# Kernel tuning notes

Hardware: AMD Instinct MI355X
Metric: run time of the kernel (lower is better)

Reference implementation:

```python
import jax, jax.numpy as jnp
import numpy as np

N_HEAD = 16
HEAD_DIM = 64
NEG_INF = -1e10


def setup_inputs() -> dict:
    key = jax.random.key(0)
    k1, k2, k3 = jax.random.split(key, 3)
    B, S, D = 1, 4096, 1024
    x = jax.random.normal(k1, (B, S, D), dtype=jnp.float32)
    Wqkv = jax.random.normal(k2, (D, 3 * D), dtype=jnp.float32) * 0.02
    bqkv = jnp.zeros((3 * D,), dtype=jnp.float32)
    Wproj = jax.random.normal(k3, (D, D), dtype=jnp.float32) * 0.02
    bproj = jnp.zeros((D,), dtype=jnp.float32)
    return {"x": x, "Wqkv": Wqkv, "bqkv": bqkv, "Wproj": Wproj, "bproj": bproj}


def reference(x, Wqkv, bqkv, Wproj, bproj):
    B, S, D = x.shape
    qkv = x @ Wqkv + bqkv                      # [B, S, 3D]
    q, k, v = jnp.split(qkv, 3, axis=2)
    # split heads -> [B, H, S, Dh]
    def split_heads(t):
        return t.reshape(B, S, N_HEAD, HEAD_DIM).transpose(0, 2, 1, 3)
    q, k, v = split_heads(q), split_heads(k), split_heads(v)
    scale = 1.0 / jnp.sqrt(jnp.float32(HEAD_DIM))
    scores = jnp.einsum('bhqd,bhkd->bhqk', q, k) * scale  # [B, H, S, S]
    causal = jnp.tril(jnp.ones((S, S), dtype=bool))[None, None]
    scores = jnp.where(causal, scores, NEG_INF)
    attn = jax.nn.softmax(scores, axis=-1)
    out = jnp.einsum('bhqk,bhkd->bhqd', attn, v)          # [B, H, S, Dh]
    out = out.transpose(0, 2, 1, 3).reshape(B, S, D)       # merge heads
    return out @ Wproj + bproj
```

## Files before the change

### kernel.cpp

```cpp
#include <hip/hip_runtime.h>
#include <stdint.h>

typedef unsigned short u16;
typedef unsigned u32;
typedef __bf16 bf16x8 __attribute__((ext_vector_type(8)));
typedef float f32x4 __attribute__((ext_vector_type(4)));
typedef u32 u32x4 __attribute__((ext_vector_type(4)));

#define S_LEN 4096
#define D_MODEL 1024
#define NHEAD 16
#define HDIM 64

__device__ __forceinline__ u16 f2bf(float f) {
  unsigned u = __builtin_bit_cast(unsigned, f);
  u += 0x7fffu + ((u >> 16) & 1u);
  return (u16)(u >> 16);
}

__device__ __forceinline__ u32 cvt_pk_bf16(float lo, float hi) {
  u32 r;
  asm("v_cvt_pk_bf16_f32 %0, %1, %2" : "=v"(r) : "v"(lo), "v"(hi));
  return r;
}

__device__ __forceinline__ int swz(int row, int col) {
  return (((col >> 3) ^ (row & 7)) << 3) | (col & 7);
}

__device__ __forceinline__ int sigma64(int s) {
  int a = s >> 4;
  return ((a >> 1) << 5) | (((s >> 2) & 3) << 3) | ((a & 1) << 2) | (s & 3);
}

__device__ __forceinline__ void gload16(const void* g, void* l) {
  auto gp = reinterpret_cast<__attribute__((address_space(1))) void*>(
      reinterpret_cast<uintptr_t>(g));
  auto lp = reinterpret_cast<__attribute__((address_space(3))) void*>(
      static_cast<unsigned>(reinterpret_cast<uintptr_t>(l)));
  __builtin_amdgcn_global_load_lds(gp, lp, 16, 0, 0);
}

__global__ __launch_bounds__(256) void k_conv(const float* __restrict__ in,
                                              u16* __restrict__ out, int n) {
  int i = (blockIdx.x * 256 + threadIdx.x) * 4;
  if (i >= n) return;
  float4 v = *reinterpret_cast<const float4*>(in + i);
  ushort4 o = make_ushort4(f2bf(v.x), f2bf(v.y), f2bf(v.z), f2bf(v.w));
  *reinterpret_cast<ushort4*>(out + i) = o;
}

__global__ __launch_bounds__(256) void k_transpose_conv(const float* __restrict__ in,
                                                        u16* __restrict__ out,
                                                        int R, int C) {
  __shared__ float tile[32][33];
  int c0 = blockIdx.x * 32, r0 = blockIdx.y * 32;
  int tx = threadIdx.x, ty = threadIdx.y;
#pragma unroll
  for (int j = 0; j < 4; ++j)
    tile[ty + j * 8][tx] = in[(size_t)(r0 + ty + j * 8) * C + c0 + tx];
  __syncthreads();
#pragma unroll
  for (int j = 0; j < 4; ++j)
    out[(size_t)(c0 + ty + j * 8) * R + r0 + tx] = f2bf(tile[tx][ty + j * 8]);
}

template <int MODE>
__global__ __launch_bounds__(256) void k_gemm(
    const u16* __restrict__ A, const u16* __restrict__ Bt,
    const float* __restrict__ bias, float* __restrict__ Cf,
    u16* __restrict__ Qd, u16* __restrict__ Kd, u16* __restrict__ Vtd,
    int M, int N, int K) {
  __shared__ __align__(16) u16 lds[2][2 * 128 * 32];
  const int tid = threadIdx.x;
  const int w = tid >> 6, lane = tid & 63;
  const int m0 = blockIdx.y * 128, n0 = blockIdx.x * 128;
  const u16* Atile = A + (size_t)m0 * K;
  const u16* Btile = Bt + (size_t)n0 * K;
  const int r = tid >> 2, c = (tid & 3) * 8;
  const int wm = (w >> 1) * 64, wn = (w & 1) * 64;

  f32x4 acc[4][4] = {};
  const int NT = K / 32;

  {
    const u16* ga = Atile + (size_t)r * K + c;
    const u16* gb = Btile + (size_t)r * K + c;
    u16* lb = lds[0];
    gload16(ga, lb + w * 512);
    gload16(ga + (size_t)64 * K, lb + 2048 + w * 512);
    gload16(gb, lb + 4096 + w * 512);
    gload16(gb + (size_t)64 * K, lb + 4096 + 2048 + w * 512);
  }
  int cur = 0;
  for (int t = 0; t < NT; ++t) {
    __syncthreads();
    if (t + 1 < NT) {
      const u16* ga = Atile + (size_t)r * K + (t + 1) * 32 + c;
      const u16* gb = Btile + (size_t)r * K + (t + 1) * 32 + c;
      u16* lb = lds[cur ^ 1];
      gload16(ga, lb + w * 512);
      gload16(ga + (size_t)64 * K, lb + 2048 + w * 512);
      gload16(gb, lb + 4096 + w * 512);
      gload16(gb + (size_t)64 * K, lb + 4096 + 2048 + w * 512);
    }
    const u16* lA = lds[cur];
    const u16* lB = lds[cur] + 4096;
    bf16x8 af[4], bfv[4];
#pragma unroll
    for (int mi = 0; mi < 4; ++mi)
      af[mi] = *reinterpret_cast<const bf16x8*>(
          lA + (wm + mi * 16 + (lane & 15)) * 32 + (lane >> 4) * 8);
#pragma unroll
    for (int ni = 0; ni < 4; ++ni)
      bfv[ni] = *reinterpret_cast<const bf16x8*>(
          lB + (wn + ni * 16 + (lane & 15)) * 32 + (lane >> 4) * 8);
#pragma unroll
    for (int mi = 0; mi < 4; ++mi)
#pragma unroll
      for (int ni = 0; ni < 4; ++ni)
        acc[mi][ni] = __builtin_amdgcn_mfma_f32_16x16x32_bf16(af[mi], bfv[ni],
                                                              acc[mi][ni], 0, 0, 0);
    cur ^= 1;
  }
#pragma unroll
  for (int mi = 0; mi < 4; ++mi) {
#pragma unroll
    for (int ni = 0; ni < 4; ++ni) {
      int colg = n0 + wn + ni * 16 + (lane & 15);
      float bv = bias[colg];
#pragma unroll
      for (int rr = 0; rr < 4; ++rr) {
        int rowg = m0 + wm + mi * 16 + ((lane >> 4) << 2) + rr;
        float v = acc[mi][ni][rr] + bv;
        if (MODE == 1) {
          Cf[(size_t)rowg * N + colg] = v;
        } else {
          if (colg < D_MODEL) {
            u16 b = f2bf(v * 0.1803368801111f);
            int hh = colg >> 6, dd = colg & 63;
            Qd[((size_t)hh * S_LEN + rowg) * 64 + swz(rowg, dd)] = b;
          } else if (colg < 2 * D_MODEL) {
            u16 b = f2bf(v);
            int cc = colg - D_MODEL;
            int hh = cc >> 6, dd = cc & 63;
            Kd[((size_t)hh * S_LEN + rowg) * 64 + swz(rowg, dd)] = b;
          } else {
            u16 b = f2bf(v);
            int cc = colg - 2 * D_MODEL;
            int hh = cc >> 6, dd = cc & 63;
            int csl = sigma64(rowg & 63);
            Vtd[((size_t)hh * 64 + dd) * S_LEN + (rowg & ~63) + swz(dd, csl)] = b;
          }
        }
      }
    }
  }
}

__global__ __launch_bounds__(256) void k_flash(const u16* __restrict__ Qd,
                                               const u16* __restrict__ Kd,
                                               const u16* __restrict__ Vtd,
                                               u16* __restrict__ Ao) {
  __shared__ __align__(16) u16 Ks[2][64 * 64];
  __shared__ __align__(16) u16 Vs[2][64 * 64];
  const int tid = threadIdx.x, w = tid >> 6, lane = tid & 63;
  const int bid = blockIdx.x;
  const int qt = 63 - (bid >> 4), h = bid & 15;
  const u16* Qh = Qd + (size_t)h * S_LEN * 64;
  const u16* Kh = Kd + (size_t)h * S_LEN * 64;
  const u16* Vh = Vtd + (size_t)h * 64 * S_LEN;
  const int r8 = tid >> 3, c8 = (tid & 7) * 8;
  const int g = lane >> 4, ql = lane & 15;

  {
    const u16* gk = Kh + (size_t)r8 * 64 + c8;
    gload16(gk, Ks[0] + w * 512);
    gload16(gk + 32 * 64, Ks[0] + 2048 + w * 512);
    const u16* gv = Vh + (size_t)r8 * S_LEN + c8;
    gload16(gv, Vs[0] + w * 512);
    gload16(gv + (size_t)32 * S_LEN, Vs[0] + 2048 + w * 512);
  }

  bf16x8 qa[2];
  {
    const int rq = qt * 64 + w * 16 + ql;
#pragma unroll
    for (int kk = 0; kk < 2; ++kk)
      qa[kk] = *reinterpret_cast<const bf16x8*>(
          Qh + (size_t)rq * 64 + swz(rq, kk * 32 + g * 8));
  }

  float m_run = -1e30f, l_part = 0.f;
  f32x4 oacc[4] = {};

  __syncthreads();

  int cur = 0;
  for (int j = 0; j <= qt; ++j) {
    if (j < qt) {
      const u16* gk = Kh + ((size_t)((j + 1) * 64 + r8)) * 64 + c8;
      gload16(gk, Ks[cur ^ 1] + w * 512);
      gload16(gk + 32 * 64, Ks[cur ^ 1] + 2048 + w * 512);
      const u16* gv = Vh + (size_t)r8 * S_LEN + (j + 1) * 64 + c8;
      gload16(gv, Vs[cur ^ 1] + w * 512);
      gload16(gv + (size_t)32 * S_LEN, Vs[cur ^ 1] + 2048 + w * 512);
    }

    f32x4 sacc[4] = {};
#pragma unroll
    for (int kk = 0; kk < 2; ++kk) {
#pragma unroll
      for (int ni = 0; ni < 4; ++ni) {
        const int kvl = ni * 16 + ql;
        bf16x8 kb = *reinterpret_cast<const bf16x8*>(
            Ks[cur] + kvl * 64 + swz(kvl, kk * 32 + g * 8));
        sacc[ni] = __builtin_amdgcn_mfma_f32_16x16x32_bf16(kb, qa[kk], sacc[ni], 0, 0, 0);
      }
    }

    float pvv[4][4];
#pragma unroll
    for (int ni = 0; ni < 4; ++ni)
#pragma unroll
      for (int rr = 0; rr < 4; ++rr) pvv[ni][rr] = sacc[ni][rr];

    if (j == qt) {
      const int qoff = w * 16 + ql;
#pragma unroll
      for (int ni = 0; ni < 4; ++ni)
#pragma unroll
        for (int rr = 0; rr < 4; ++rr)
          if (ni * 16 + g * 4 + rr > qoff) pvv[ni][rr] = -1e30f;
    }

    float mx;
    {
      float a0 = fmaxf(fmaxf(pvv[0][0], pvv[0][1]), fmaxf(pvv[0][2], pvv[0][3]));
      float a1 = fmaxf(fmaxf(pvv[1][0], pvv[1][1]), fmaxf(pvv[1][2], pvv[1][3]));
      float a2 = fmaxf(fmaxf(pvv[2][0], pvv[2][1]), fmaxf(pvv[2][2], pvv[2][3]));
      float a3 = fmaxf(fmaxf(pvv[3][0], pvv[3][1]), fmaxf(pvv[3][2], pvv[3][3]));
      mx = fmaxf(fmaxf(a0, a1), fmaxf(a2, a3));
      mx = fmaxf(mx, __shfl_xor(mx, 16));
      mx = fmaxf(mx, __shfl_xor(mx, 32));
    }

    if (__any(mx > m_run + 8.f)) {
      float mn = fmaxf(m_run, mx);
      float alpha = exp2f(m_run - mn);
      m_run = mn;
      l_part *= alpha;
      float ao[4];
#pragma unroll
      for (int rr = 0; rr < 4; ++rr) ao[rr] = __shfl(alpha, g * 4 + rr);
#pragma unroll
      for (int ni = 0; ni < 4; ++ni)
#pragma unroll
        for (int rr = 0; rr < 4; ++rr) oacc[ni][rr] *= ao[rr];
    }

    u32 pk[4][2];
    {
      float rs = 0.f;
#pragma unroll
      for (int ni = 0; ni < 4; ++ni) {
        float p0 = exp2f(pvv[ni][0] - m_run);
        float p1 = exp2f(pvv[ni][1] - m_run);
        float p2 = exp2f(pvv[ni][2] - m_run);
        float p3 = exp2f(pvv[ni][3] - m_run);
        rs += (p0 + p1) + (p2 + p3);
        pk[ni][0] = cvt_pk_bf16(p0, p1);
        pk[ni][1] = cvt_pk_bf16(p2, p3);
      }
      l_part += rs;
    }

#pragma unroll
    for (int kk2 = 0; kk2 < 2; ++kk2) {
      u32x4 pw = {pk[2 * kk2][0], pk[2 * kk2][1], pk[2 * kk2 + 1][0], pk[2 * kk2 + 1][1]};
      bf16x8 pa = __builtin_bit_cast(bf16x8, pw);
#pragma unroll
      for (int ni = 0; ni < 4; ++ni) {
        const int dd = ni * 16 + ql;
        bf16x8 vb = *reinterpret_cast<const bf16x8*>(
            Vs[cur] + dd * 64 + swz(dd, kk2 * 32 + g * 8));
        oacc[ni] = __builtin_amdgcn_mfma_f32_16x16x32_bf16(pa, vb, oacc[ni], 0, 0, 0);
      }
    }

    __syncthreads();
    cur ^= 1;
  }

  {
    float l = l_part;
    l += __shfl_xor(l, 16);
    l += __shfl_xor(l, 32);
    float inv = 1.f / l;
    float io[4];
#pragma unroll
    for (int rr = 0; rr < 4; ++rr) io[rr] = __shfl(inv, g * 4 + rr);
#pragma unroll
    for (int rr = 0; rr < 4; ++rr) {
      int rowg = qt * 64 + w * 16 + g * 4 + rr;
#pragma unroll
      for (int ni = 0; ni < 4; ++ni) {
        int colg = h * 64 + ni * 16 + ql;
        Ao[(size_t)rowg * D_MODEL + colg] = f2bf(oacc[ni][rr] * io[rr]);
      }
    }
  }
}

extern "C" void kernel_launch(void* const* d_in, const int* in_sizes, int n_in,
                              void* d_out, int out_size, void* d_ws, size_t ws_size,
                              hipStream_t stream) {
  const float* x = (const float*)d_in[0];
  const float* Wqkv = (const float*)d_in[1];
  const float* bqkv = (const float*)d_in[2];
  const float* Wproj = (const float*)d_in[3];
  const float* bproj = (const float*)d_in[4];
  float* out = (float*)d_out;
  char* ws = (char*)d_ws;

  u16* xb = (u16*)(ws);
  u16* aout = (u16*)(ws);
  u16* wqkvt = (u16*)(ws + (size_t)(8 << 20));
  u16* wprojt = (u16*)(ws + (size_t)(14 << 20));
  u16* Qd = (u16*)(ws + (size_t)(16 << 20));
  u16* Kd = (u16*)(ws + (size_t)(24 << 20));
  u16* Vtd = (u16*)(ws + (size_t)(32 << 20));

  if (ws_size < (size_t)(40 << 20)) return;

  k_conv<<<dim3(4096), dim3(256), 0, stream>>>(x, xb, S_LEN * D_MODEL);
  k_transpose_conv<<<dim3(96, 32), dim3(32, 8), 0, stream>>>(Wqkv, wqkvt, D_MODEL,
                                                             3 * D_MODEL);
  k_transpose_conv<<<dim3(32, 32), dim3(32, 8), 0, stream>>>(Wproj, wprojt, D_MODEL,
                                                             D_MODEL);
  k_gemm<0><<<dim3(24, 32), dim3(256), 0, stream>>>(xb, wqkvt, bqkv, nullptr, Qd, Kd,
                                                    Vtd, S_LEN, 3 * D_MODEL, D_MODEL);
  k_flash<<<dim3(1024), dim3(256), 0, stream>>>(Qd, Kd, Vtd, aout);
  k_gemm<1><<<dim3(8, 32), dim3(256), 0, stream>>>(aout, wprojt, bproj, out, nullptr,
                                                   nullptr, nullptr, S_LEN, D_MODEL,
                                                   D_MODEL);
}
```

Baseline: 226.9 us.

## Pair causal query tiles per block and use narrower-N GEMM for projection

The flash kernel now has each block process two query tiles, i and 63-i, sharing the K/V loads for the first i+1 tiles. This balances causal work across 512 uniform blocks instead of 1024 uneven ones. The output projection switches to a new 128x64-tile GEMM that launches 512 blocks instead of 256, for better CU coverage. The trade-off is more registers per thread for the second accumulator set, and only 512 flash blocks, which may cost occupancy.

```diff
diff --git a/kernel.cpp b/kernel.cpp
--- a/kernel.cpp
+++ b/kernel.cpp
@@ -158,6 +158,162 @@
   }
 }
 
+__global__ __launch_bounds__(256) void k_gemm_n64(
+    const u16* __restrict__ A, const u16* __restrict__ Bt,
+    const float* __restrict__ bias, float* __restrict__ Cf,
+    int M, int N, int K) {
+  __shared__ __align__(16) u16 lds[2][(128 + 64) * 32];
+  const int tid = threadIdx.x;
+  const int w = tid >> 6, lane = tid & 63;
+  const int g = lane >> 4, ql = lane & 15;
+  const int m0 = blockIdx.y * 128, n0 = blockIdx.x * 64;
+  const u16* Atile = A + (size_t)m0 * K;
+  const u16* Btile = Bt + (size_t)n0 * K;
+  const int r = tid >> 2, c = (tid & 3) * 8;
+  const int wm = (w >> 1) * 64, wn = (w & 1) * 32;
+
+  f32x4 acc[4][2] = {};
+  const int NT = K / 32;
+
+  {
+    const u16* ga = Atile + (size_t)r * K + c;
+    const u16* gb = Btile + (size_t)r * K + c;
+    u16* lb = lds[0];
+    gload16(ga, lb + w * 512);
+    gload16(ga + (size_t)64 * K, lb + 2048 + w * 512);
+    gload16(gb, lb + 4096 + w * 512);
+  }
+  int cur = 0;
+  for (int t = 0; t < NT; ++t) {
+    __syncthreads();
+    if (t + 1 < NT) {
+      const u16* ga = Atile + (size_t)r * K + (t + 1) * 32 + c;
+      const u16* gb = Btile + (size_t)r * K + (t + 1) * 32 + c;
+      u16* lb = lds[cur ^ 1];
+      gload16(ga, lb + w * 512);
+      gload16(ga + (size_t)64 * K, lb + 2048 + w * 512);
+      gload16(gb, lb + 4096 + w * 512);
+    }
+    const u16* lA = lds[cur];
+    const u16* lB = lds[cur] + 4096;
+    bf16x8 af[4], bfv[2];
+#pragma unroll
+    for (int mi = 0; mi < 4; ++mi)
+      af[mi] = *reinterpret_cast<const bf16x8*>(
+          lA + (wm + mi * 16 + ql) * 32 + g * 8);
+#pragma unroll
+    for (int ni = 0; ni < 2; ++ni)
+      bfv[ni] = *reinterpret_cast<const bf16x8*>(
+          lB + (wn + ni * 16 + ql) * 32 + g * 8);
+#pragma unroll
+    for (int mi = 0; mi < 4; ++mi)
+#pragma unroll
+      for (int ni = 0; ni < 2; ++ni)
+        acc[mi][ni] = __builtin_amdgcn_mfma_f32_16x16x32_bf16(af[mi], bfv[ni],
+                                                              acc[mi][ni], 0, 0, 0);
+    cur ^= 1;
+  }
+#pragma unroll
+  for (int mi = 0; mi < 4; ++mi)
+#pragma unroll
+    for (int ni = 0; ni < 2; ++ni) {
+      int colg = n0 + wn + ni * 16 + ql;
+      float bv = bias[colg];
+#pragma unroll
+      for (int rr = 0; rr < 4; ++rr) {
+        int rowg = m0 + wm + mi * 16 + g * 4 + rr;
+        Cf[(size_t)rowg * N + colg] = acc[mi][ni][rr] + bv;
+      }
+    }
+}
+
+__device__ __forceinline__ void flash_tile(const u16* __restrict__ Ksb,
+                                           const u16* __restrict__ Vsb,
+                                           bf16x8 qa0, bf16x8 qa1,
+                                           float& m_run, float& l_part,
+                                           f32x4* oacc, int g, int ql, int qoff,
+                                           bool diag) {
+  f32x4 sacc[4] = {};
+#pragma unroll
+  for (int kk = 0; kk < 2; ++kk) {
+    bf16x8 qk = kk ? qa1 : qa0;
+#pragma unroll
+    for (int ni = 0; ni < 4; ++ni) {
+      const int kvl = ni * 16 + ql;
+      bf16x8 kb = *reinterpret_cast<const bf16x8*>(
+          Ksb + kvl * 64 + swz(kvl, kk * 32 + g * 8));
+      sacc[ni] = __builtin_amdgcn_mfma_f32_16x16x32_bf16(kb, qk, sacc[ni], 0, 0, 0);
+    }
+  }
+  float pvv[4][4];
+#pragma unroll
+  for (int ni = 0; ni < 4; ++ni)
+#pragma unroll
+    for (int rr = 0; rr < 4; ++rr) pvv[ni][rr] = sacc[ni][rr];
+
+  if (diag) {
+#pragma unroll
+    for (int ni = 0; ni < 4; ++ni)
+#pragma unroll
+      for (int rr = 0; rr < 4; ++rr)
+        if (ni * 16 + g * 4 + rr > qoff) pvv[ni][rr] = -1e30f;
+  }
+
+  float mx;
+  {
+    float a0 = fmaxf(fmaxf(pvv[0][0], pvv[0][1]), fmaxf(pvv[0][2], pvv[0][3]));
+    float a1 = fmaxf(fmaxf(pvv[1][0], pvv[1][1]), fmaxf(pvv[1][2], pvv[1][3]));
+    float a2 = fmaxf(fmaxf(pvv[2][0], pvv[2][1]), fmaxf(pvv[2][2], pvv[2][3]));
+    float a3 = fmaxf(fmaxf(pvv[3][0], pvv[3][1]), fmaxf(pvv[3][2], pvv[3][3]));
+    mx = fmaxf(fmaxf(a0, a1), fmaxf(a2, a3));
+    mx = fmaxf(mx, __shfl_xor(mx, 16));
+    mx = fmaxf(mx, __shfl_xor(mx, 32));
+  }
+
+  if (__any(mx > m_run + 8.f)) {
+    float mn = fmaxf(m_run, mx);
+    float alpha = exp2f(m_run - mn);
+    m_run = mn;
+    l_part *= alpha;
+    float ao[4];
+#pragma unroll
+    for (int rr = 0; rr < 4; ++rr) ao[rr] = __shfl(alpha, g * 4 + rr);
+#pragma unroll
+    for (int ni = 0; ni < 4; ++ni)
+#pragma unroll
+      for (int rr = 0; rr < 4; ++rr) oacc[ni][rr] *= ao[rr];
+  }
+
+  u32 pk[4][2];
+  {
+    float rs = 0.f;
+#pragma unroll
+    for (int ni = 0; ni < 4; ++ni) {
+      float p0 = exp2f(pvv[ni][0] - m_run);
+      float p1 = exp2f(pvv[ni][1] - m_run);
+      float p2 = exp2f(pvv[ni][2] - m_run);
+      float p3 = exp2f(pvv[ni][3] - m_run);
+      rs += (p0 + p1) + (p2 + p3);
+      pk[ni][0] = cvt_pk_bf16(p0, p1);
+      pk[ni][1] = cvt_pk_bf16(p2, p3);
+    }
+    l_part += rs;
+  }
+
+#pragma unroll
+  for (int kk2 = 0; kk2 < 2; ++kk2) {
+    u32x4 pw = {pk[2 * kk2][0], pk[2 * kk2][1], pk[2 * kk2 + 1][0], pk[2 * kk2 + 1][1]};
+    bf16x8 pa = __builtin_bit_cast(bf16x8, pw);
+#pragma unroll
+    for (int ni = 0; ni < 4; ++ni) {
+      const int dd = ni * 16 + ql;
+      bf16x8 vb = *reinterpret_cast<const bf16x8*>(
+          Vsb + dd * 64 + swz(dd, kk2 * 32 + g * 8));
+      oacc[ni] = __builtin_amdgcn_mfma_f32_16x16x32_bf16(pa, vb, oacc[ni], 0, 0, 0);
+    }
+  }
+}
+
 __global__ __launch_bounds__(256) void k_flash(const u16* __restrict__ Qd,
                                                const u16* __restrict__ Kd,
                                                const u16* __restrict__ Vtd,
@@ -166,12 +322,14 @@
   __shared__ __align__(16) u16 Vs[2][64 * 64];
   const int tid = threadIdx.x, w = tid >> 6, lane = tid & 63;
   const int bid = blockIdx.x;
-  const int qt = 63 - (bid >> 4), h = bid & 15;
+  const int i = bid >> 4, h = bid & 15;
+  const int J = 63 - i;
   const u16* Qh = Qd + (size_t)h * S_LEN * 64;
   const u16* Kh = Kd + (size_t)h * S_LEN * 64;
   const u16* Vh = Vtd + (size_t)h * 64 * S_LEN;
   const int r8 = tid >> 3, c8 = (tid & 7) * 8;
   const int g = lane >> 4, ql = lane & 15;
+  const int qoff = w * 16 + ql;
 
   {
     const u16* gk = Kh + (size_t)r8 * 64 + c8;
@@ -182,23 +340,27 @@
     gload16(gv + (size_t)32 * S_LEN, Vs[0] + 2048 + w * 512);
   }
 
-  bf16x8 qa[2];
-  {
-    const int rq = qt * 64 + w * 16 + ql;
-#pragma unroll
-    for (int kk = 0; kk < 2; ++kk)
-      qa[kk] = *reinterpret_cast<const bf16x8*>(
-          Qh + (size_t)rq * 64 + swz(rq, kk * 32 + g * 8));
-  }
-
-  float m_run = -1e30f, l_part = 0.f;
-  f32x4 oacc[4] = {};
+  bf16x8 qaA[2], qaB[2];
+  {
+    const int rqA = J * 64 + w * 16 + ql;
+    const int rqB = i * 64 + w * 16 + ql;
+#pragma unroll
+    for (int kk = 0; kk < 2; ++kk) {
+      qaA[kk] = *reinterpret_cast<const bf16x8*>(
+          Qh + (size_t)rqA * 64 + swz(rqA, kk * 32 + g * 8));
+      qaB[kk] = *reinterpret_cast<const bf16x8*>(
+          Qh + (size_t)rqB * 64 + swz(rqB, kk * 32 + g * 8));
+    }
+  }
+
+  float mA = -1e30f, lA = 0.f, mB = -1e30f, lB = 0.f;
+  f32x4 oA[4] = {}, oB[4] = {};
 
   __syncthreads();
 
   int cur = 0;
-  for (int j = 0; j <= qt; ++j) {
-    if (j < qt) {
+  for (int j = 0; j <= i; ++j) {
+    {
       const u16* gk = Kh + ((size_t)((j + 1) * 64 + r8)) * 64 + c8;
       gload16(gk, Ks[cur ^ 1] + w * 512);
       gload16(gk + 32 * 64, Ks[cur ^ 1] + 2048 + w * 512);
@@ -206,94 +368,30 @@
       gload16(gv, Vs[cur ^ 1] + w * 512);
       gload16(gv + (size_t)32 * S_LEN, Vs[cur ^ 1] + 2048 + w * 512);
     }
-
-    f32x4 sacc[4] = {};
-#pragma unroll
-    for (int kk = 0; kk < 2; ++kk) {
-#pragma unroll
-      for (int ni = 0; ni < 4; ++ni) {
-        const int kvl = ni * 16 + ql;
-        bf16x8 kb = *reinterpret_cast<const bf16x8*>(
-            Ks[cur] + kvl * 64 + swz(kvl, kk * 32 + g * 8));
-        sacc[ni] = __builtin_amdgcn_mfma_f32_16x16x32_bf16(kb, qa[kk], sacc[ni], 0, 0, 0);
-      }
-    }
-
-    float pvv[4][4];
-#pragma unroll
-    for (int ni = 0; ni < 4; ++ni)
-#pragma unroll
-      for (int rr = 0; rr < 4; ++rr) pvv[ni][rr] = sacc[ni][rr];
-
-    if (j == qt) {
-      const int qoff = w * 16 + ql;
-#pragma unroll
-      for (int ni = 0; ni < 4; ++ni)
-#pragma unroll
-        for (int rr = 0; rr < 4; ++rr)
-          if (ni * 16 + g * 4 + rr > qoff) pvv[ni][rr] = -1e30f;
-    }
-
-    float mx;
-    {
-      float a0 = fmaxf(fmaxf(pvv[0][0], pvv[0][1]), fmaxf(pvv[0][2], pvv[0][3]));
-      float a1 = fmaxf(fmaxf(pvv[1][0], pvv[1][1]), fmaxf(pvv[1][2], pvv[1][3]));
-      float a2 = fmaxf(fmaxf(pvv[2][0], pvv[2][1]), fmaxf(pvv[2][2], pvv[2][3]));
-      float a3 = fmaxf(fmaxf(pvv[3][0], pvv[3][1]), fmaxf(pvv[3][2], pvv[3][3]));
-      mx = fmaxf(fmaxf(a0, a1), fmaxf(a2, a3));
-      mx = fmaxf(mx, __shfl_xor(mx, 16));
-      mx = fmaxf(mx, __shfl_xor(mx, 32));
-    }
-
-    if (__any(mx > m_run + 8.f)) {
-      float mn = fmaxf(m_run, mx);
-      float alpha = exp2f(m_run - mn);
-      m_run = mn;
-      l_part *= alpha;
-      float ao[4];
-#pragma unroll
-      for (int rr = 0; rr < 4; ++rr) ao[rr] = __shfl(alpha, g * 4 + rr);
-#pragma unroll
-      for (int ni = 0; ni < 4; ++ni)
-#pragma unroll
-        for (int rr = 0; rr < 4; ++rr) oacc[ni][rr] *= ao[rr];
-    }
-
-    u32 pk[4][2];
-    {
-      float rs = 0.f;
-#pragma unroll
-      for (int ni = 0; ni < 4; ++ni) {
-        float p0 = exp2f(pvv[ni][0] - m_run);
-        float p1 = exp2f(pvv[ni][1] - m_run);
-        float p2 = exp2f(pvv[ni][2] - m_run);
-        float p3 = exp2f(pvv[ni][3] - m_run);
-        rs += (p0 + p1) + (p2 + p3);
-        pk[ni][0] = cvt_pk_bf16(p0, p1);
-        pk[ni][1] = cvt_pk_bf16(p2, p3);
-      }
-      l_part += rs;
-    }
-
-#pragma unroll
-    for (int kk2 = 0; kk2 < 2; ++kk2) {
-      u32x4 pw = {pk[2 * kk2][0], pk[2 * kk2][1], pk[2 * kk2 + 1][0], pk[2 * kk2 + 1][1]};
-      bf16x8 pa = __builtin_bit_cast(bf16x8, pw);
-#pragma unroll
-      for (int ni = 0; ni < 4; ++ni) {
-        const int dd = ni * 16 + ql;
-        bf16x8 vb = *reinterpret_cast<const bf16x8*>(
-            Vs[cur] + dd * 64 + swz(dd, kk2 * 32 + g * 8));
-        oacc[ni] = __builtin_amdgcn_mfma_f32_16x16x32_bf16(pa, vb, oacc[ni], 0, 0, 0);
-      }
-    }
-
+    flash_tile(Ks[cur], Vs[cur], qaA[0], qaA[1], mA, lA, oA, g, ql, qoff, false);
+    flash_tile(Ks[cur], Vs[cur], qaB[0], qaB[1], mB, lB, oB, g, ql, qoff, j == i);
     __syncthreads();
     cur ^= 1;
   }
-
-  {
-    float l = l_part;
+  for (int j = i + 1; j <= J; ++j) {
+    if (j < J) {
+      const u16* gk = Kh + ((size_t)((j + 1) * 64 + r8)) * 64 + c8;
+      gload16(gk, Ks[cur ^ 1] + w * 512);
+      gload16(gk + 32 * 64, Ks[cur ^ 1] + 2048 + w * 512);
+      const u16* gv = Vh + (size_t)r8 * S_LEN + (j + 1) * 64 + c8;
+      gload16(gv, Vs[cur ^ 1] + w * 512);
+      gload16(gv + (size_t)32 * S_LEN, Vs[cur ^ 1] + 2048 + w * 512);
+    }
+    flash_tile(Ks[cur], Vs[cur], qaA[0], qaA[1], mA, lA, oA, g, ql, qoff, j == J);
+    __syncthreads();
+    cur ^= 1;
+  }
+
+#pragma unroll
+  for (int t = 0; t < 2; ++t) {
+    float l = t ? lB : lA;
+    f32x4* oacc = t ? oB : oA;
+    int qt = t ? i : J;
     l += __shfl_xor(l, 16);
     l += __shfl_xor(l, 32);
     float inv = 1.f / l;
@@ -340,8 +438,7 @@
                                                              D_MODEL);
   k_gemm<0><<<dim3(24, 32), dim3(256), 0, stream>>>(xb, wqkvt, bqkv, nullptr, Qd, Kd,
                                                     Vtd, S_LEN, 3 * D_MODEL, D_MODEL);
-  k_flash<<<dim3(1024), dim3(256), 0, stream>>>(Qd, Kd, Vtd, aout);
-  k_gemm<1><<<dim3(8, 32), dim3(256), 0, stream>>>(aout, wprojt, bproj, out, nullptr,
-                                                   nullptr, nullptr, S_LEN, D_MODEL,
-                                                   D_MODEL);
-}
+  k_flash<<<dim3(512), dim3(256), 0, stream>>>(Qd, Kd, Vtd, aout);
+  k_gemm_n64<<<dim3(16, 32), dim3(256), 0, stream>>>(aout, wprojt, bproj, out, S_LEN,
+                                                     D_MODEL, D_MODEL);
+}
```

Result: no change. 224.3 us (-1.2%).
